# Kernel tuning notes

Hardware: AMD Instinct MI355X
Metric: run time of the kernel (lower is better)

Reference implementation:

```python
import jax, jax.numpy as jnp
import numpy as np

B, L, D, H = 8, 1024, 512, 8  # batch, seq, d_model, n_head (per-head dim == d_model)
EPS = 1e-6


def setup_inputs() -> dict:
    key = jax.random.key(0)
    ks = jax.random.split(key, 7)
    s = 1.0 / np.sqrt(D)
    return {
        "q": jax.random.normal(ks[0], (B, L, D), jnp.float32),
        "k": jax.random.normal(ks[1], (B, L, D), jnp.float32),
        "v": jax.random.normal(ks[2], (B, L, D), jnp.float32),
        "w_q": jax.random.normal(ks[3], (D, H * D), jnp.float32) * s,
        "w_k": jax.random.normal(ks[4], (D, H * D), jnp.float32) * s,
        "w_v": jax.random.normal(ks[5], (D, H * D), jnp.float32) * s,
        "w_fc": jax.random.normal(ks[6], (H * D, D), jnp.float32) * (1.0 / np.sqrt(H * D)),
        "ln_gamma": jnp.ones((D,), jnp.float32),
        "ln_beta": jnp.zeros((D,), jnp.float32),
    }


def reference(q, k, v, w_q, w_k, w_v, w_fc, ln_gamma, ln_beta):
    residual = q
    # projections -> (B, H, L, D); dropout is identity in eval mode
    qh = (q @ w_q).reshape(B, L, H, D).transpose(0, 2, 1, 3)
    kh = (k @ w_k).reshape(B, L, H, D).transpose(0, 2, 1, 3)
    vh = (v @ w_v).reshape(B, L, H, D).transpose(0, 2, 1, 3)
    temp = jnp.asarray(D, qh.dtype) ** 0.5
    scores = jnp.einsum("bhqd,bhkd->bhqk", qh / temp, kh)
    attn = jax.nn.softmax(scores, axis=-1)
    ctx = jnp.einsum("bhqk,bhkd->bhqd", attn, vh)
    ctx = ctx.transpose(0, 2, 1, 3).reshape(B, L, H * D)
    out = ctx @ w_fc + residual
    mu = jnp.mean(out, axis=-1, keepdims=True)
    var = jnp.var(out, axis=-1, keepdims=True)
    out = (out - mu) * jax.lax.rsqrt(var + EPS) * ln_gamma + ln_beta
    return out, attn
```

## Files before the change

kernel.cpp:

```cpp
#include <hip/hip_runtime.h>
#include <hip/hip_bf16.h>
#include <math.h>

typedef __bf16 bf16_t;
typedef __bf16 bf16x8 __attribute__((ext_vector_type(8)));
typedef __bf16 bf16x4 __attribute__((ext_vector_type(4)));
typedef float  f32x4  __attribute__((ext_vector_type(4)));

#define B_   8
#define L_   1024
#define D_   512
#define H_   8
#define HD_  4096
#define BL_  8192

__device__ __forceinline__ void gload_lds16(const bf16_t* g, bf16_t* l) {
  __builtin_amdgcn_global_load_lds(
      (const __attribute__((address_space(1))) unsigned int*)g,
      (__attribute__((address_space(3))) unsigned int*)l,
      16, 0, 0);
}

__global__ void f2b(const float4* __restrict__ s, bf16x4* __restrict__ d, int n4) {
  int i = blockIdx.x * blockDim.x + threadIdx.x;
  if (i >= n4) return;
  float4 v = s[i];
  bf16x4 o;
  o[0] = (bf16_t)v.x; o[1] = (bf16_t)v.y; o[2] = (bf16_t)v.z; o[3] = (bf16_t)v.w;
  d[i] = o;
}

__global__ void tconv(const float* __restrict__ s, bf16_t* __restrict__ d, int R, int C) {
  __shared__ float t[32][33];
  int c0 = blockIdx.x * 32, r0 = blockIdx.y * 32;
  int tx = threadIdx.x, ty = threadIdx.y;
  #pragma unroll
  for (int i = 0; i < 32; i += 8)
    t[ty + i][tx] = s[(long)(r0 + ty + i) * C + c0 + tx];
  __syncthreads();
  #pragma unroll
  for (int i = 0; i < 32; i += 8)
    d[(long)(c0 + ty + i) * R + r0 + tx] = (bf16_t)t[tx][ty + i];
}

__global__ void tbf(const bf16_t* __restrict__ s, bf16_t* __restrict__ d) {
  __shared__ bf16_t t[32][33];
  int bz = blockIdx.z; int b = bz >> 3, h = bz & 7;
  const bf16_t* S = s + (long)b * L_ * HD_ + (long)h * D_;
  bf16_t* Dp = d + (long)bz * D_ * L_;
  int l0 = blockIdx.y * 32, d0 = blockIdx.x * 32;
  int tx = threadIdx.x, ty = threadIdx.y;
  #pragma unroll
  for (int i = 0; i < 32; i += 8)
    t[ty + i][tx] = S[(long)(l0 + ty + i) * HD_ + d0 + tx];
  __syncthreads();
  #pragma unroll
  for (int i = 0; i < 32; i += 8)
    Dp[(long)(d0 + ty + i) * L_ + l0 + tx] = t[tx][ty + i];
}


#define VM4 asm volatile("s_waitcnt vmcnt(4)" ::: "memory")
#define VM0 asm volatile("s_waitcnt vmcnt(0)" ::: "memory")

#define STG(OP, BUF, KK, TILE) do { \
  const bf16_t* gsrc_ = (OP) ? Bg : Ag; \
  const long gld_ = (OP) ? ldb : lda; \
  bf16_t* lb_ = lds + (BUF)*32768 + (OP)*16384 + (KK)*8192 + wid*512; \
  gload_lds16(gsrc_ + (long)(TILE)*64 + (KK)*32, lb_); \
  gload_lds16(gsrc_ + (long)128*gld_ + (long)(TILE)*64 + (KK)*32, lb_ + 4096); \
} while (0)

#define LDA(I, BUF, KK) (*(const bf16x8*)(lds + (BUF)*32768 + (KK)*8192 + offA[I]))
#define LDB(J, BUF, KK) (*(const bf16x8*)(lds + (BUF)*32768 + 16384 + (KK)*8192 + offB[J]))

#define MM(q, ii, jj) acc[(q)*4+(ii)][(jj)] = \
  __builtin_amdgcn_mfma_f32_16x16x32_bf16(a##ii, b##jj, acc[(q)*4+(ii)][(jj)], 0, 0, 0)

#define PHASE(Q, KK, BUF, STAGE, VM) do { \
  bf16x8 a0, a1, a2, a3; \
  if ((Q) == 0) { b0 = LDB(0,BUF,KK); b1 = LDB(1,BUF,KK); b2 = LDB(2,BUF,KK); b3 = LDB(3,BUF,KK); } \
  a0 = LDA((Q)*4+0,BUF,KK); a1 = LDA((Q)*4+1,BUF,KK); \
  a2 = LDA((Q)*4+2,BUF,KK); a3 = LDA((Q)*4+3,BUF,KK); \
  STAGE; \
  __builtin_amdgcn_s_barrier(); \
  asm volatile("s_waitcnt lgkmcnt(0)" ::: "memory"); \
  __builtin_amdgcn_sched_barrier(0); \
  __builtin_amdgcn_s_setprio(1); \
  MM(Q,0,0); MM(Q,1,0); MM(Q,2,0); MM(Q,3,0); \
  MM(Q,0,1); MM(Q,1,1); MM(Q,2,1); MM(Q,3,1); \
  MM(Q,0,2); MM(Q,1,2); MM(Q,2,2); MM(Q,3,2); \
  MM(Q,0,3); MM(Q,1,3); MM(Q,2,3); MM(Q,3,3); \
  __builtin_amdgcn_s_setprio(0); \
  VM; \
  __builtin_amdgcn_s_barrier(); \
} while (0)

template<int EPI>
__launch_bounds__(512, 2)
__global__ void gemm256(const bf16_t* __restrict__ A, long sAb, long sAh, int lda,
                        const bf16_t* __restrict__ Bt, long sBb, long sBh, int ldb,
                        void* __restrict__ Cv, long sCb, long sCh, int ldc,
                        int K, float scale)
{
  __shared__ __align__(16) bf16_t lds[65536];
  const int bz = blockIdx.z, b = bz >> 3, h = bz & 7;
  A  += (long)b * sAb + (long)h * sAh;
  Bt += (long)b * sBb + (long)h * sBh;
  const int m0 = blockIdx.y * 256, n0 = blockIdx.x * 256;
  const int tid = threadIdx.x, lane = tid & 63, wid = tid >> 6;
  const int wm = wid >> 2, wn = wid & 3;

  const int srow  = tid >> 2;
  const int sslot = (lane & 3) ^ ((tid >> 3) & 3);
  const bf16_t* Ag = A + (long)(m0 + srow) * lda + sslot * 8;
  const bf16_t* Bg = Bt + (long)(n0 + srow) * ldb + sslot * 8;

  int offA[8], offB[4];
  #pragma unroll
  for (int i = 0; i < 8; ++i) {
    const int r = wm * 128 + i * 16 + (lane & 15);
    offA[i] = r * 32 + (((lane >> 4) ^ ((r >> 1) & 3)) * 8);
  }
  #pragma unroll
  for (int j = 0; j < 4; ++j) {
    const int r = wn * 64 + j * 16 + (lane & 15);
    offB[j] = r * 32 + (((lane >> 4) ^ ((r >> 1) & 3)) * 8);
  }

  f32x4 acc[8][4] = {};
  const int ITER = K >> 7;

  STG(0,0,0,0); STG(0,0,1,0); STG(1,0,0,0); STG(1,0,1,0);
  STG(0,1,0,1); STG(1,1,0,1);
  VM4;
  __builtin_amdgcn_s_barrier();

  for (int i = 0; i < ITER; ++i) {
    const int t = 2 * i;
    const bool stg = (i + 1 < ITER);
    bf16x8 b0, b1, b2, b3;
    PHASE(0,0,0, STG(0,1,1,t+1);                , (void)0);
    PHASE(1,0,0, STG(1,1,1,t+1);                , (void)0);
    PHASE(0,1,0, { if (stg) STG(0,0,0,t+2); }   , (void)0);
    PHASE(1,1,0, { if (stg) STG(1,0,0,t+2); }   , { if (stg) { VM4; } else { VM0; } });
    PHASE(0,0,1, { if (stg) STG(0,0,1,t+2); }   , (void)0);
    PHASE(1,0,1, { if (stg) STG(1,0,1,t+2); }   , (void)0);
    PHASE(0,1,1, { if (stg) STG(0,1,0,t+3); }   , (void)0);
    PHASE(1,1,1, { if (stg) STG(1,1,0,t+3); }   , { if (stg) { VM4; } });
  }

  const long coff = (long)b * sCb + (long)h * sCh;
  #pragma unroll
  for (int i = 0; i < 8; ++i) {
    const int rbase = m0 + wm * 128 + i * 16 + ((lane >> 4) << 2);
    #pragma unroll
    for (int j = 0; j < 4; ++j) {
      const int c = n0 + wn * 64 + j * 16 + (lane & 15);
      #pragma unroll
      for (int r = 0; r < 4; ++r) {
        float vv = acc[i][j][r] * scale;
        long idx = coff + (long)(rbase + r) * ldc + c;
        if (EPI == 0) ((bf16_t*)Cv)[idx] = (bf16_t)vv;
        else          ((float*)Cv)[idx] = vv;
      }
    }
  }
}

template<int BM, int BN, int EPI>
__launch_bounds__(256, 2)
__global__ void gemm_bt(const bf16_t* __restrict__ A, long sAb, long sAh, int lda,
                        const bf16_t* __restrict__ Bt, long sBb, long sBh, int ldb,
                        void* __restrict__ Cv, long sCb, long sCh, int ldc,
                        int K, float scale, const float* __restrict__ res)
{
  constexpr int WN    = (BN == 128) ? 2 : 1;
  constexpr int SPANM = BM / (4 / WN);
  constexpr int MI    = SPANM / 16;
  constexpr int NJ    = 4;
  __shared__ bf16_t sA[BM * 64];
  __shared__ bf16_t sB[BN * 64];
  const int bz = blockIdx.z, b = bz >> 3, h = bz & 7;
  A  += (long)b * sAb + (long)h * sAh;
  Bt += (long)b * sBb + (long)h * sBh;
  const int m0 = blockIdx.y * BM, n0 = blockIdx.x * BN;
  const int tid = threadIdx.x, lane = tid & 63, wid = tid >> 6;
  const int waveM = (WN == 2) ? (wid >> 1) : wid;
  const int waveN = (WN == 2) ? (wid & 1) : 0;
  f32x4 acc[MI][NJ] = {};
  const int srow = wid * 8 + (lane >> 3);
  const int skin = (lane & 7) * 8;
  const bf16_t* Ag = A + (long)(m0 + srow) * lda + skin;
  const bf16_t* Bg = Bt + (long)(n0 + srow) * ldb + skin;
  for (int k0 = 0; k0 < K; k0 += 64) {
    #pragma unroll
    for (int j = 0; j < BM / 32; ++j)
      gload_lds16(Ag + (long)(j * 32) * lda + k0, sA + (j * 4 + wid) * 512);
    #pragma unroll
    for (int j = 0; j < BN / 32; ++j)
      gload_lds16(Bg + (long)(j * 32) * ldb + k0, sB + (j * 4 + wid) * 512);
    __syncthreads();
    #pragma unroll
    for (int kk = 0; kk < 2; ++kk) {
      bf16x8 af[MI], bfr[NJ];
      #pragma unroll
      for (int i = 0; i < MI; ++i)
        af[i]  = *(const bf16x8*)(sA + (waveM * SPANM + i * 16 + (lane & 15)) * 64 + kk * 32 + ((lane >> 4) * 8));
      #pragma unroll
      for (int j = 0; j < NJ; ++j)
        bfr[j] = *(const bf16x8*)(sB + (waveN * 64 + j * 16 + (lane & 15)) * 64 + kk * 32 + ((lane >> 4) * 8));
      #pragma unroll
      for (int i = 0; i < MI; ++i)
        #pragma unroll
        for (int j = 0; j < NJ; ++j)
          acc[i][j] = __builtin_amdgcn_mfma_f32_16x16x32_bf16(af[i], bfr[j], acc[i][j], 0, 0, 0);
    }
    __syncthreads();
  }
  const long coff = (long)b * sCb + (long)h * sCh;
  #pragma unroll
  for (int i = 0; i < MI; ++i) {
    const int rbase = m0 + waveM * SPANM + i * 16 + ((lane >> 4) << 2);
    #pragma unroll
    for (int j = 0; j < NJ; ++j) {
      const int c = n0 + waveN * 64 + j * 16 + (lane & 15);
      #pragma unroll
      for (int r = 0; r < 4; ++r) {
        float v = acc[i][j][r] * scale;
        long idx = coff + (long)(rbase + r) * ldc + c;
        if (EPI == 0)      ((bf16_t*)Cv)[idx] = (bf16_t)v;
        else if (EPI == 1) ((float*)Cv)[idx] = v;
        else               ((float*)Cv)[idx] = v + res[(long)(rbase + r) * ldc + c];
      }
    }
  }
}

__global__ void softmax_rows(float* __restrict__ attn, bf16_t* __restrict__ abf) {
  const long row = (long)blockIdx.x * 4 + (threadIdx.x >> 6);
  const int lane = threadIdx.x & 63;
  float* p = attn + row * 1024;
  float4 v[4];
  float m = -1e30f;
  #pragma unroll
  for (int j = 0; j < 4; ++j) {
    v[j] = ((const float4*)p)[j * 64 + lane];
    m = fmaxf(m, fmaxf(fmaxf(v[j].x, v[j].y), fmaxf(v[j].z, v[j].w)));
  }
  #pragma unroll
  for (int o = 32; o; o >>= 1) m = fmaxf(m, __shfl_xor(m, o));
  float s = 0.f;
  #pragma unroll
  for (int j = 0; j < 4; ++j) {
    v[j].x = expf(v[j].x - m); v[j].y = expf(v[j].y - m);
    v[j].z = expf(v[j].z - m); v[j].w = expf(v[j].w - m);
    s += v[j].x + v[j].y + v[j].z + v[j].w;
  }
  #pragma unroll
  for (int o = 32; o; o >>= 1) s += __shfl_xor(s, o);
  const float inv = 1.f / s;
  bf16x4* ab = (bf16x4*)(abf + row * 1024);
  #pragma unroll
  for (int j = 0; j < 4; ++j) {
    v[j].x *= inv; v[j].y *= inv; v[j].z *= inv; v[j].w *= inv;
    ((float4*)p)[j * 64 + lane] = v[j];
    bf16x4 o4;
    o4[0] = (bf16_t)v[j].x; o4[1] = (bf16_t)v[j].y;
    o4[2] = (bf16_t)v[j].z; o4[3] = (bf16_t)v[j].w;
    ab[j * 64 + lane] = o4;
  }
}

__global__ void ln_rows(float* __restrict__ o, const float* __restrict__ g,
                        const float* __restrict__ be) {
  const long row = (long)blockIdx.x * 4 + (threadIdx.x >> 6);
  const int lane = threadIdx.x & 63;
  float* p = o + row * 512;
  float4 a = ((const float4*)p)[lane];
  float4 b = ((const float4*)p)[lane + 64];
  float s  = a.x + a.y + a.z + a.w + b.x + b.y + b.z + b.w;
  float s2 = a.x*a.x + a.y*a.y + a.z*a.z + a.w*a.w
           + b.x*b.x + b.y*b.y + b.z*b.z + b.w*b.w;
  #pragma unroll
  for (int t = 32; t; t >>= 1) { s += __shfl_xor(s, t); s2 += __shfl_xor(s2, t); }
  const float mu  = s * (1.f / 512.f);
  const float var = s2 * (1.f / 512.f) - mu * mu;
  const float inv = rsqrtf(var + 1e-6f);
  float4 g0 = ((const float4*)g)[lane],  g1 = ((const float4*)g)[lane + 64];
  float4 b0 = ((const float4*)be)[lane], b1 = ((const float4*)be)[lane + 64];
  a.x = (a.x - mu) * inv * g0.x + b0.x;  a.y = (a.y - mu) * inv * g0.y + b0.y;
  a.z = (a.z - mu) * inv * g0.z + b0.z;  a.w = (a.w - mu) * inv * g0.w + b0.w;
  b.x = (b.x - mu) * inv * g1.x + b1.x;  b.y = (b.y - mu) * inv * g1.y + b1.y;
  b.z = (b.z - mu) * inv * g1.z + b1.z;  b.w = (b.w - mu) * inv * g1.w + b1.w;
  ((float4*)p)[lane] = a;
  ((float4*)p)[lane + 64] = b;
}

extern "C" void kernel_launch(void* const* d_in, const int* in_sizes, int n_in,
                              void* d_out, int out_size, void* d_ws, size_t ws_size,
                              hipStream_t stream) {
  const float* q   = (const float*)d_in[0];
  const float* k   = (const float*)d_in[1];
  const float* v   = (const float*)d_in[2];
  const float* wq  = (const float*)d_in[3];
  const float* wk  = (const float*)d_in[4];
  const float* wv  = (const float*)d_in[5];
  const float* wfc = (const float*)d_in[6];
  const float* lng = (const float*)d_in[7];
  const float* lnb = (const float*)d_in[8];

  float* out   = (float*)d_out;
  float* attnf = out + (long)BL_ * D_;

  char* ws = (char*)d_ws;
  const long MB = 1024 * 1024;
  bf16_t* qbf = (bf16_t*)(ws +   0 * MB);
  bf16_t* kbf = (bf16_t*)(ws +   8 * MB);
  bf16_t* vbf = (bf16_t*)(ws +  16 * MB);
  bf16_t* wqT = (bf16_t*)(ws +  24 * MB);
  bf16_t* wkT = (bf16_t*)(ws +  28 * MB);
  bf16_t* wvT = (bf16_t*)(ws +  32 * MB);
  bf16_t* wfT = (bf16_t*)(ws +  36 * MB);
  bf16_t* qh  = (bf16_t*)(ws +  40 * MB);
  bf16_t* kh  = (bf16_t*)(ws + 104 * MB);
  bf16_t* vh  = (bf16_t*)(ws + 168 * MB);
  bf16_t* vhT = (bf16_t*)(ws + 232 * MB);
  bf16_t* abf = qh;
  bf16_t* ctx = vh;

  const int n4 = BL_ * D_ / 4;
  f2b<<<dim3(n4 / 256), 256, 0, stream>>>((const float4*)q, (bf16x4*)qbf, n4);
  f2b<<<dim3(n4 / 256), 256, 0, stream>>>((const float4*)k, (bf16x4*)kbf, n4);
  f2b<<<dim3(n4 / 256), 256, 0, stream>>>((const float4*)v, (bf16x4*)vbf, n4);
  tconv<<<dim3(HD_ / 32, D_ / 32), dim3(32, 8), 0, stream>>>(wq,  wqT, D_, HD_);
  tconv<<<dim3(HD_ / 32, D_ / 32), dim3(32, 8), 0, stream>>>(wk,  wkT, D_, HD_);
  tconv<<<dim3(HD_ / 32, D_ / 32), dim3(32, 8), 0, stream>>>(wv,  wvT, D_, HD_);
  tconv<<<dim3(D_ / 32, HD_ / 32), dim3(32, 8), 0, stream>>>(wfc, wfT, HD_, D_);

  const float qscale = 1.0f / sqrtf((float)D_);
  gemm256<0><<<dim3(16, 32, 1), 512, 0, stream>>>(qbf, 0, 0, D_, wqT, 0, 0, D_,
                                                  qh, 0, 0, HD_, D_, qscale);
  gemm256<0><<<dim3(16, 32, 1), 512, 0, stream>>>(kbf, 0, 0, D_, wkT, 0, 0, D_,
                                                  kh, 0, 0, HD_, D_, 1.0f);
  gemm256<0><<<dim3(16, 32, 1), 512, 0, stream>>>(vbf, 0, 0, D_, wvT, 0, 0, D_,
                                                  vh, 0, 0, HD_, D_, 1.0f);

  tbf<<<dim3(D_ / 32, L_ / 32, B_ * H_), dim3(32, 8), 0, stream>>>(vh, vhT);

  gemm256<1><<<dim3(4, 4, B_ * H_), 512, 0, stream>>>(
      qh, (long)L_ * HD_, D_, HD_,
      kh, (long)L_ * HD_, D_, HD_,
      attnf, (long)H_ * L_ * L_, (long)L_ * L_, L_, D_, 1.0f);

  softmax_rows<<<dim3(B_ * H_ * L_ / 4), 256, 0, stream>>>(attnf, abf);

  gemm256<0><<<dim3(2, 4, B_ * H_), 512, 0, stream>>>(
      abf, (long)H_ * L_ * L_, (long)L_ * L_, L_,
      vhT, (long)H_ * D_ * L_, (long)D_ * L_, L_,
      ctx, (long)L_ * HD_, D_, HD_, L_, 1.0f);

  gemm_bt<128,64,2><<<dim3(8, 64, 1), 256, 0, stream>>>(
      ctx, 0, 0, HD_, wfT, 0, 0, HD_,
      out, 0, 0, D_, HD_, 1.0f, q);

  ln_rows<<<dim3(BL_ / 4), 256, 0, stream>>>(out, lng, lnb);
}
```

Measured before the change: 646.1 us.

## Fuse QK^T score GEMM with row softmax; merge q/k/v bf16 conversions

Adds a kernel that computes a full 32x1024 score block per workgroup (all of K streamed through LDS), then does the row softmax in registers and writes both fp32 attn and the bf16 copy. This removes the fp32 score write and re-read by a separate softmax pass. The three fp32-to-bf16 input conversions are also merged into one launch. The fused path is used only when the workspace is large enough for a separate bf16 attn buffer. It trades the tiled GEMM's reuse for a narrow 32-row tile that rereads K per query tile and uses large LDS, which limits occupancy.

```diff
diff --git a/kernel.cpp b/kernel.cpp
--- a/kernel.cpp
+++ b/kernel.cpp
@@ -21,12 +21,16 @@
       16, 0, 0);
 }
 
-__global__ void f2b(const float4* __restrict__ s, bf16x4* __restrict__ d, int n4) {
+__global__ void f2b3(const float4* __restrict__ q, const float4* __restrict__ k,
+                     const float4* __restrict__ v, bf16x4* __restrict__ qo,
+                     bf16x4* __restrict__ ko, bf16x4* __restrict__ vo, int n4) {
   int i = blockIdx.x * blockDim.x + threadIdx.x;
   if (i >= n4) return;
-  float4 v = s[i];
+  const float4* s = (blockIdx.y == 0) ? q : (blockIdx.y == 1) ? k : v;
+  bf16x4* d = (blockIdx.y == 0) ? qo : (blockIdx.y == 1) ? ko : vo;
+  float4 x = s[i];
   bf16x4 o;
-  o[0] = (bf16_t)v.x; o[1] = (bf16_t)v.y; o[2] = (bf16_t)v.z; o[3] = (bf16_t)v.w;
+  o[0] = (bf16_t)x.x; o[1] = (bf16_t)x.y; o[2] = (bf16_t)x.z; o[3] = (bf16_t)x.w;
   d[i] = o;
 }
 
@@ -58,7 +62,6 @@
   for (int i = 0; i < 32; i += 8)
     Dp[(long)(d0 + ty + i) * L_ + l0 + tx] = t[tx][ty + i];
 }
-
 
 #define VM4 asm volatile("s_waitcnt vmcnt(4)" ::: "memory")
 #define VM0 asm volatile("s_waitcnt vmcnt(0)" ::: "memory")
@@ -237,6 +240,107 @@
   }
 }
 
+__launch_bounds__(512, 2)
+__global__ void smsm(const bf16_t* __restrict__ qh, const bf16_t* __restrict__ kh,
+                     float* __restrict__ attn, bf16_t* __restrict__ abf)
+{
+  __shared__ __align__(16) bf16_t sK[1024 * 32];
+  __shared__ __align__(16) bf16_t sQ[32 * 32];
+  __shared__ float st[2][4][32];
+  const int qt = blockIdx.x, bh = blockIdx.y;
+  const int b = bh >> 3, h = bh & 7;
+  const bf16_t* Ab = qh + ((long)b * L_ + qt * 32) * HD_ + h * D_;
+  const bf16_t* Bb = kh + (long)b * L_ * HD_ + h * D_;
+  const int tid = threadIdx.x, lane = tid & 63, wid = tid >> 6;
+  const int wq = wid >> 2, wk = wid & 3;
+  const int g = lane >> 4, fr = lane & 15;
+  const int sCol = ((tid & 3) ^ ((tid >> 4) & 3)) * 8;
+  const bf16_t* Ag = Ab + (long)(tid >> 2) * HD_ + sCol;
+  const bf16_t* Bg = Bb + (long)(tid >> 2) * HD_ + sCol;
+  const int rsw = (g ^ (fr >> 2)) * 16;
+  const int offA = (wq * 16 + fr) * 64 + rsw;
+  const int offB0 = (wk * 256 + fr) * 64 + rsw;
+
+  f32x4 acc[16] = {};
+  for (int k0 = 0; k0 < D_; k0 += 32) {
+    if (wid < 2) gload_lds16(Ag + k0, sQ + wid * 512);
+    #pragma unroll
+    for (int j = 0; j < 8; ++j)
+      gload_lds16(Bg + (long)j * 128 * HD_ + k0, sK + j * 4096 + wid * 512);
+    __syncthreads();
+    bf16x8 af = *(const bf16x8*)((const char*)sQ + offA);
+    #pragma unroll
+    for (int jj = 0; jj < 4; ++jj) {
+      bf16x8 b0 = *(const bf16x8*)((const char*)sK + offB0 + (jj * 4 + 0) * 1024);
+      bf16x8 b1 = *(const bf16x8*)((const char*)sK + offB0 + (jj * 4 + 1) * 1024);
+      bf16x8 b2 = *(const bf16x8*)((const char*)sK + offB0 + (jj * 4 + 2) * 1024);
+      bf16x8 b3 = *(const bf16x8*)((const char*)sK + offB0 + (jj * 4 + 3) * 1024);
+      acc[jj*4+0] = __builtin_amdgcn_mfma_f32_16x16x32_bf16(af, b0, acc[jj*4+0], 0, 0, 0);
+      acc[jj*4+1] = __builtin_amdgcn_mfma_f32_16x16x32_bf16(af, b1, acc[jj*4+1], 0, 0, 0);
+      acc[jj*4+2] = __builtin_amdgcn_mfma_f32_16x16x32_bf16(af, b2, acc[jj*4+2], 0, 0, 0);
+      acc[jj*4+3] = __builtin_amdgcn_mfma_f32_16x16x32_bf16(af, b3, acc[jj*4+3], 0, 0, 0);
+    }
+    __syncthreads();
+  }
+
+  const int rbase = wq * 16 + g * 4;
+  float mx[4] = {-1e30f, -1e30f, -1e30f, -1e30f};
+  #pragma unroll
+  for (int j = 0; j < 16; ++j)
+    #pragma unroll
+    for (int r = 0; r < 4; ++r) mx[r] = fmaxf(mx[r], acc[j][r]);
+  #pragma unroll
+  for (int r = 0; r < 4; ++r) {
+    float v = mx[r];
+    v = fmaxf(v, __shfl_xor(v, 1)); v = fmaxf(v, __shfl_xor(v, 2));
+    v = fmaxf(v, __shfl_xor(v, 4)); v = fmaxf(v, __shfl_xor(v, 8));
+    mx[r] = v;
+  }
+  if (fr == 0)
+    #pragma unroll
+    for (int r = 0; r < 4; ++r) st[0][wk][rbase + r] = mx[r];
+  __syncthreads();
+  float m[4], sum[4] = {0.f, 0.f, 0.f, 0.f};
+  #pragma unroll
+  for (int r = 0; r < 4; ++r)
+    m[r] = fmaxf(fmaxf(st[0][0][rbase + r], st[0][1][rbase + r]),
+                 fmaxf(st[0][2][rbase + r], st[0][3][rbase + r]));
+  #pragma unroll
+  for (int j = 0; j < 16; ++j)
+    #pragma unroll
+    for (int r = 0; r < 4; ++r) {
+      float p = __expf(acc[j][r] - m[r]);
+      acc[j][r] = p;
+      sum[r] += p;
+    }
+  #pragma unroll
+  for (int r = 0; r < 4; ++r) {
+    float v = sum[r];
+    v += __shfl_xor(v, 1); v += __shfl_xor(v, 2);
+    v += __shfl_xor(v, 4); v += __shfl_xor(v, 8);
+    sum[r] = v;
+  }
+  if (fr == 0)
+    #pragma unroll
+    for (int r = 0; r < 4; ++r) st[1][wk][rbase + r] = sum[r];
+  __syncthreads();
+  float inv[4];
+  #pragma unroll
+  for (int r = 0; r < 4; ++r)
+    inv[r] = 1.f / (st[1][0][rbase + r] + st[1][1][rbase + r] +
+                    st[1][2][rbase + r] + st[1][3][rbase + r]);
+  const long idx0 = (long)bh * L_ * L_ + (long)(qt * 32 + rbase) * L_ + wk * 256 + fr;
+  #pragma unroll
+  for (int j = 0; j < 16; ++j)
+    #pragma unroll
+    for (int r = 0; r < 4; ++r) {
+      float p = acc[j][r] * inv[r];
+      long idx = idx0 + (long)r * L_ + j * 16;
+      attn[idx] = p;
+      abf[idx] = (bf16_t)p;
+    }
+}
+
 __global__ void softmax_rows(float* __restrict__ attn, bf16_t* __restrict__ abf) {
   const long row = (long)blockIdx.x * 4 + (threadIdx.x >> 6);
   const int lane = threadIdx.x & 63;
@@ -326,13 +430,16 @@
   bf16_t* kh  = (bf16_t*)(ws + 104 * MB);
   bf16_t* vh  = (bf16_t*)(ws + 168 * MB);
   bf16_t* vhT = (bf16_t*)(ws + 232 * MB);
-  bf16_t* abf = qh;
   bf16_t* ctx = vh;
 
+  const bool fused = (ws_size >= (size_t)(424 * MB));
+  bf16_t* abf = fused ? (bf16_t*)(ws + 296 * MB)
+                      : qh;
+
   const int n4 = BL_ * D_ / 4;
-  f2b<<<dim3(n4 / 256), 256, 0, stream>>>((const float4*)q, (bf16x4*)qbf, n4);
-  f2b<<<dim3(n4 / 256), 256, 0, stream>>>((const float4*)k, (bf16x4*)kbf, n4);
-  f2b<<<dim3(n4 / 256), 256, 0, stream>>>((const float4*)v, (bf16x4*)vbf, n4);
+  f2b3<<<dim3(n4 / 256, 3), 256, 0, stream>>>((const float4*)q, (const float4*)k,
+                                              (const float4*)v, (bf16x4*)qbf,
+                                              (bf16x4*)kbf, (bf16x4*)vbf, n4);
   tconv<<<dim3(HD_ / 32, D_ / 32), dim3(32, 8), 0, stream>>>(wq,  wqT, D_, HD_);
   tconv<<<dim3(HD_ / 32, D_ / 32), dim3(32, 8), 0, stream>>>(wk,  wkT, D_, HD_);
   tconv<<<dim3(HD_ / 32, D_ / 32), dim3(32, 8), 0, stream>>>(wv,  wvT, D_, HD_);
@@ -348,12 +455,15 @@
 
   tbf<<<dim3(D_ / 32, L_ / 32, B_ * H_), dim3(32, 8), 0, stream>>>(vh, vhT);
 
-  gemm256<1><<<dim3(4, 4, B_ * H_), 512, 0, stream>>>(
-      qh, (long)L_ * HD_, D_, HD_,
-      kh, (long)L_ * HD_, D_, HD_,
-      attnf, (long)H_ * L_ * L_, (long)L_ * L_, L_, D_, 1.0f);
-
-  softmax_rows<<<dim3(B_ * H_ * L_ / 4), 256, 0, stream>>>(attnf, abf);
+  if (fused) {
+    smsm<<<dim3(L_ / 32, B_ * H_), 512, 0, stream>>>(qh, kh, attnf, abf);
+  } else {
+    gemm256<1><<<dim3(4, 4, B_ * H_), 512, 0, stream>>>(
+        qh, (long)L_ * HD_, D_, HD_,
+        kh, (long)L_ * HD_, D_, HD_,
+        attnf, (long)H_ * L_ * L_, (long)L_ * L_, L_, D_, 1.0f);
+    softmax_rows<<<dim3(B_ * H_ * L_ / 4), 256, 0, stream>>>(attnf, abf);
+  }
 
   gemm256<0><<<dim3(2, 4, B_ * H_), 512, 0, stream>>>(
       abf, (long)H_ * L_ * L_, (long)L_ * L_, L_,
```

Result: slower. 684.2 us (+5.9%).

## Fuse conversion launches, write V transposed from GEMM, and store scores in bf16

Applied to the files above, without the earlier changes.

Merges the three input-conversion launches and the four weight-transpose launches into one launch each. The V projection GEMM gets a new epilogue that writes the per-head transposed layout directly, which removes the separate transpose kernel. When the workspace is large enough, the QK^T scores are stored as bf16 and a new softmax reads them and writes both the fp32 attention output and the bf16 probabilities in place. This cuts fp32 round-trip traffic on the scores, but rounding the logits to bf16 before softmax lowers accuracy, and the epilogue's strided 8-byte transposed stores may coalesce poorly.

```diff
diff --git a/kernel.cpp b/kernel.cpp
--- a/kernel.cpp
+++ b/kernel.cpp
@@ -21,18 +21,34 @@
       16, 0, 0);
 }
 
-__global__ void f2b(const float4* __restrict__ s, bf16x4* __restrict__ d, int n4) {
+__global__ void f2b3(const float4* __restrict__ q, const float4* __restrict__ k,
+                     const float4* __restrict__ v, bf16x4* __restrict__ qo,
+                     bf16x4* __restrict__ ko, bf16x4* __restrict__ vo, int n4) {
   int i = blockIdx.x * blockDim.x + threadIdx.x;
   if (i >= n4) return;
-  float4 v = s[i];
+  const float4* s = (blockIdx.y == 0) ? q : (blockIdx.y == 1) ? k : v;
+  bf16x4* d = (blockIdx.y == 0) ? qo : (blockIdx.y == 1) ? ko : vo;
+  float4 x = s[i];
   bf16x4 o;
-  o[0] = (bf16_t)v.x; o[1] = (bf16_t)v.y; o[2] = (bf16_t)v.z; o[3] = (bf16_t)v.w;
+  o[0] = (bf16_t)x.x; o[1] = (bf16_t)x.y; o[2] = (bf16_t)x.z; o[3] = (bf16_t)x.w;
   d[i] = o;
 }
 
-__global__ void tconv(const float* __restrict__ s, bf16_t* __restrict__ d, int R, int C) {
+__global__ void tconv4(const float* __restrict__ wq, const float* __restrict__ wk,
+                       const float* __restrict__ wv, const float* __restrict__ wfc,
+                       bf16_t* __restrict__ wqT, bf16_t* __restrict__ wkT,
+                       bf16_t* __restrict__ wvT, bf16_t* __restrict__ wfT) {
   __shared__ float t[32][33];
-  int c0 = blockIdx.x * 32, r0 = blockIdx.y * 32;
+  const int z = blockIdx.z;
+  const float* s; bf16_t* d; int R, C, c0, r0;
+  if (z < 3) {
+    s = (z == 0) ? wq : (z == 1) ? wk : wv;
+    d = (z == 0) ? wqT : (z == 1) ? wkT : wvT;
+    R = D_; C = HD_; c0 = blockIdx.x * 32; r0 = blockIdx.y * 32;
+  } else {
+    s = wfc; d = wfT;
+    R = HD_; C = D_; c0 = blockIdx.y * 32; r0 = blockIdx.x * 32;
+  }
   int tx = threadIdx.x, ty = threadIdx.y;
   #pragma unroll
   for (int i = 0; i < 32; i += 8)
@@ -42,23 +58,6 @@
   for (int i = 0; i < 32; i += 8)
     d[(long)(c0 + ty + i) * R + r0 + tx] = (bf16_t)t[tx][ty + i];
 }
-
-__global__ void tbf(const bf16_t* __restrict__ s, bf16_t* __restrict__ d) {
-  __shared__ bf16_t t[32][33];
-  int bz = blockIdx.z; int b = bz >> 3, h = bz & 7;
-  const bf16_t* S = s + (long)b * L_ * HD_ + (long)h * D_;
-  bf16_t* Dp = d + (long)bz * D_ * L_;
-  int l0 = blockIdx.y * 32, d0 = blockIdx.x * 32;
-  int tx = threadIdx.x, ty = threadIdx.y;
-  #pragma unroll
-  for (int i = 0; i < 32; i += 8)
-    t[ty + i][tx] = S[(long)(l0 + ty + i) * HD_ + d0 + tx];
-  __syncthreads();
-  #pragma unroll
-  for (int i = 0; i < 32; i += 8)
-    Dp[(long)(d0 + ty + i) * L_ + l0 + tx] = t[tx][ty + i];
-}
-
 
 #define VM4 asm volatile("s_waitcnt vmcnt(4)" ::: "memory")
 #define VM0 asm volatile("s_waitcnt vmcnt(0)" ::: "memory")
@@ -157,12 +156,21 @@
     #pragma unroll
     for (int j = 0; j < 4; ++j) {
       const int c = n0 + wn * 64 + j * 16 + (lane & 15);
-      #pragma unroll
-      for (int r = 0; r < 4; ++r) {
-        float vv = acc[i][j][r] * scale;
-        long idx = coff + (long)(rbase + r) * ldc + c;
-        if (EPI == 0) ((bf16_t*)Cv)[idx] = (bf16_t)vv;
-        else          ((float*)Cv)[idx] = vv;
+      if (EPI == 3) {
+        const int b2 = rbase >> 10, l2 = rbase & 1023;
+        const int h2 = c >> 9, d2 = c & 511;
+        bf16x4 o4;
+        #pragma unroll
+        for (int r = 0; r < 4; ++r) o4[r] = (bf16_t)(acc[i][j][r] * scale);
+        *(bf16x4*)((bf16_t*)Cv + (long)(b2 * 8 + h2) * D_ * L_ + (long)d2 * L_ + l2) = o4;
+      } else {
+        #pragma unroll
+        for (int r = 0; r < 4; ++r) {
+          float vv = acc[i][j][r] * scale;
+          long idx = coff + (long)(rbase + r) * ldc + c;
+          if (EPI == 0) ((bf16_t*)Cv)[idx] = (bf16_t)vv;
+          else          ((float*)Cv)[idx] = vv;
+        }
       }
     }
   }
@@ -237,6 +245,41 @@
   }
 }
 
+__global__ void softmax_bf16(bf16_t* __restrict__ braw, float* __restrict__ attn) {
+  const long row = (long)blockIdx.x * 4 + (threadIdx.x >> 6);
+  const int lane = threadIdx.x & 63;
+  bf16_t* p = braw + row * 1024;
+  float* ao = attn + row * 1024;
+  float v[16];
+  float m = -1e30f;
+  #pragma unroll
+  for (int j = 0; j < 4; ++j) {
+    bf16x4 x = *(const bf16x4*)(p + j * 256 + lane * 4);
+    #pragma unroll
+    for (int e = 0; e < 4; ++e) {
+      v[j * 4 + e] = (float)x[e];
+      m = fmaxf(m, v[j * 4 + e]);
+    }
+  }
+  #pragma unroll
+  for (int o = 32; o; o >>= 1) m = fmaxf(m, __shfl_xor(m, o));
+  float s = 0.f;
+  #pragma unroll
+  for (int e = 0; e < 16; ++e) { v[e] = __expf(v[e] - m); s += v[e]; }
+  #pragma unroll
+  for (int o = 32; o; o >>= 1) s += __shfl_xor(s, o);
+  const float inv = 1.f / s;
+  #pragma unroll
+  for (int j = 0; j < 4; ++j) {
+    float4 f; bf16x4 o4;
+    f.x = v[j*4+0] * inv; f.y = v[j*4+1] * inv;
+    f.z = v[j*4+2] * inv; f.w = v[j*4+3] * inv;
+    o4[0] = (bf16_t)f.x; o4[1] = (bf16_t)f.y; o4[2] = (bf16_t)f.z; o4[3] = (bf16_t)f.w;
+    ((float4*)ao)[j * 64 + lane] = f;
+    *(bf16x4*)(p + j * 256 + lane * 4) = o4;
+  }
+}
+
 __global__ void softmax_rows(float* __restrict__ attn, bf16_t* __restrict__ abf) {
   const long row = (long)blockIdx.x * 4 + (threadIdx.x >> 6);
   const int lane = threadIdx.x & 63;
@@ -326,34 +369,40 @@
   bf16_t* kh  = (bf16_t*)(ws + 104 * MB);
   bf16_t* vh  = (bf16_t*)(ws + 168 * MB);
   bf16_t* vhT = (bf16_t*)(ws + 232 * MB);
-  bf16_t* abf = qh;
   bf16_t* ctx = vh;
 
+  const bool fused = (ws_size >= (size_t)(424 * MB));
+  bf16_t* braw = (bf16_t*)(ws + 296 * MB);
+  bf16_t* abf  = fused ? braw : qh;
+
   const int n4 = BL_ * D_ / 4;
-  f2b<<<dim3(n4 / 256), 256, 0, stream>>>((const float4*)q, (bf16x4*)qbf, n4);
-  f2b<<<dim3(n4 / 256), 256, 0, stream>>>((const float4*)k, (bf16x4*)kbf, n4);
-  f2b<<<dim3(n4 / 256), 256, 0, stream>>>((const float4*)v, (bf16x4*)vbf, n4);
-  tconv<<<dim3(HD_ / 32, D_ / 32), dim3(32, 8), 0, stream>>>(wq,  wqT, D_, HD_);
-  tconv<<<dim3(HD_ / 32, D_ / 32), dim3(32, 8), 0, stream>>>(wk,  wkT, D_, HD_);
-  tconv<<<dim3(HD_ / 32, D_ / 32), dim3(32, 8), 0, stream>>>(wv,  wvT, D_, HD_);
-  tconv<<<dim3(D_ / 32, HD_ / 32), dim3(32, 8), 0, stream>>>(wfc, wfT, HD_, D_);
+  f2b3<<<dim3(n4 / 256, 3), 256, 0, stream>>>((const float4*)q, (const float4*)k,
+                                              (const float4*)v, (bf16x4*)qbf,
+                                              (bf16x4*)kbf, (bf16x4*)vbf, n4);
+  tconv4<<<dim3(128, 16, 4), dim3(32, 8), 0, stream>>>(wq, wk, wv, wfc,
+                                                       wqT, wkT, wvT, wfT);
 
   const float qscale = 1.0f / sqrtf((float)D_);
   gemm256<0><<<dim3(16, 32, 1), 512, 0, stream>>>(qbf, 0, 0, D_, wqT, 0, 0, D_,
                                                   qh, 0, 0, HD_, D_, qscale);
   gemm256<0><<<dim3(16, 32, 1), 512, 0, stream>>>(kbf, 0, 0, D_, wkT, 0, 0, D_,
                                                   kh, 0, 0, HD_, D_, 1.0f);
-  gemm256<0><<<dim3(16, 32, 1), 512, 0, stream>>>(vbf, 0, 0, D_, wvT, 0, 0, D_,
-                                                  vh, 0, 0, HD_, D_, 1.0f);
-
-  tbf<<<dim3(D_ / 32, L_ / 32, B_ * H_), dim3(32, 8), 0, stream>>>(vh, vhT);
-
-  gemm256<1><<<dim3(4, 4, B_ * H_), 512, 0, stream>>>(
-      qh, (long)L_ * HD_, D_, HD_,
-      kh, (long)L_ * HD_, D_, HD_,
-      attnf, (long)H_ * L_ * L_, (long)L_ * L_, L_, D_, 1.0f);
-
-  softmax_rows<<<dim3(B_ * H_ * L_ / 4), 256, 0, stream>>>(attnf, abf);
+  gemm256<3><<<dim3(16, 32, 1), 512, 0, stream>>>(vbf, 0, 0, D_, wvT, 0, 0, D_,
+                                                  vhT, 0, 0, 0, D_, 1.0f);
+
+  if (fused) {
+    gemm256<0><<<dim3(4, 4, B_ * H_), 512, 0, stream>>>(
+        qh, (long)L_ * HD_, D_, HD_,
+        kh, (long)L_ * HD_, D_, HD_,
+        braw, (long)H_ * L_ * L_, (long)L_ * L_, L_, D_, 1.0f);
+    softmax_bf16<<<dim3(B_ * H_ * L_ / 4), 256, 0, stream>>>(braw, attnf);
+  } else {
+    gemm256<1><<<dim3(4, 4, B_ * H_), 512, 0, stream>>>(
+        qh, (long)L_ * HD_, D_, HD_,
+        kh, (long)L_ * HD_, D_, HD_,
+        attnf, (long)H_ * L_ * L_, (long)L_ * L_, L_, D_, 1.0f);
+    softmax_rows<<<dim3(B_ * H_ * L_ / 4), 256, 0, stream>>>(attnf, abf);
+  }
 
   gemm256<0><<<dim3(2, 4, B_ * H_), 512, 0, stream>>>(
       abf, (long)H_ * L_ * L_, (long)L_ * L_, L_,
```

Result: faster. 565.4 us (-12.5%).
